# Performance work log

Hardware: AMD Instinct MI355X
Metric: run time of the kernel (lower is better)

The kernel has to match this reference:

```python
import jax, jax.numpy as jnp
import numpy as np

N, E, H, L = 2000, 32000, 300, 30


def setup_inputs() -> dict:
    key = jax.random.key(0)
    ks = jax.random.split(key, 24)
    x = jax.random.normal(ks[0], (N, 4), jnp.float32)
    edge_attr = jax.random.uniform(ks[1], (E, 2), dtype=jnp.float32)
    edge_index = jax.random.randint(ks[2], (2, E), 0, N, jnp.int32)
    y = jax.random.uniform(ks[3], (E,), dtype=jnp.float32)

    def w(k, shape, fan):
        return (jax.random.normal(k, shape, jnp.float32) / np.sqrt(fan)).astype(jnp.float32)

    inp = dict(x=x, edge_attr=edge_attr, edge_index=edge_index, y=y)
    inp['node_emb_W'] = w(ks[4], (4, H), 4)
    inp['node_emb_b'] = jnp.zeros((H,), jnp.float32)
    inp['edge_d_W'] = w(ks[5], (1, H // 2), 1)
    inp['edge_d_b'] = jnp.zeros((H // 2,), jnp.float32)
    inp['edge_t_W'] = w(ks[6], (1, H // 2), 1)
    inp['edge_t_b'] = jnp.zeros((H // 2,), jnp.float32)
    # stacked per-layer params [L, ...]
    inp['eU_W'] = w(ks[7], (L, H, H), H)
    inp['eU_b'] = jnp.zeros((L, H), jnp.float32)
    inp['eW_W'] = w(ks[8], (L, H, H), H)
    inp['eW_b'] = jnp.zeros((L, H), jnp.float32)
    inp['nU_W'] = w(ks[9], (L, H, H), H)
    inp['nU_b'] = jnp.zeros((L, H), jnp.float32)
    inp['nV_W'] = w(ks[10], (L, H, H), H)
    inp['nV_b'] = jnp.zeros((L, H), jnp.float32)
    inp['bn_e_g'] = jnp.ones((L, H), jnp.float32)
    inp['bn_e_b'] = jnp.zeros((L, H), jnp.float32)
    inp['bn_n_g'] = jnp.ones((L, H), jnp.float32)
    inp['bn_n_b'] = jnp.zeros((L, H), jnp.float32)
    inp['cls_W'] = w(ks[11], (H, 1), H)
    inp['cls_b'] = jnp.zeros((1,), jnp.float32)
    return inp


def _bn(v, g, b):  # BatchNorm1d in training mode (batch statistics), eps=1e-5
    m = v.mean(0)
    var = v.var(0)
    return (v - m) * jax.lax.rsqrt(var + 1e-5) * g + b


def _forward(x, edge_attr, edge_index, y, node_emb_W, node_emb_b, edge_d_W, edge_d_b,
             edge_t_W, edge_t_b, eU_W, eU_b, eW_W, eW_b, nU_W, nU_b, nV_W, nV_b,
             bn_e_g, bn_e_b, bn_n_g, bn_n_b, cls_W, cls_b):
    src, dst = edge_index[0], edge_index[1]
    n_nodes = x.shape[0]
    node = x @ node_emb_W + node_emb_b                                  # [N, H]
    edge = jnp.concatenate([edge_attr[:, :1] @ edge_d_W + edge_d_b,
                            edge_attr[:, 1:2] @ edge_t_W + edge_t_b], axis=1)  # [E, H]

    def layer(carry, p):
        node, edge = carry
        eUW, eUb, eWW, eWb, nUW, nUb, nVW, nVb, geg, geb, gng, gnb = p
        xs = node[src]                                                  # x_j gather [E, H]
        xd = node[dst]                                                  # x_i gather [E, H]
        # edge_update: edge_U(x_j) + edge_U(x_i)  (edge_U used for both, as in source)
        edge_gate = edge @ eWW + eWb + (xs @ eUW + eUb) + (xd @ eUW + eUb)
        edge_new = edge + jax.nn.relu(_bn(edge_gate, geg, geb))
        # message: eta * node_V(x_j), with global (dim=0) sigmoid-sum normalization as in source
        sigma = jax.nn.sigmoid(edge)
        eta = sigma / (sigma.sum(0) + 1e-20)                            # [E, H] / [H]
        msg = eta * (xs @ nVW + nVb)
        agg = jax.ops.segment_sum(msg, dst, num_segments=n_nodes)       # scatter-add
        node_gate = node @ nUW + nUb + agg
        node_new = node + jax.nn.relu(_bn(node_gate, gng, gnb))
        return (node_new, edge_new), None

    (node, edge), _ = jax.lax.scan(
        layer, (node, edge),
        (eU_W, eU_b, eW_W, eW_b, nU_W, nU_b, nV_W, nV_b, bn_e_g, bn_e_b, bn_n_g, bn_n_b))

    pred = jax.nn.sigmoid(edge @ cls_W + cls_b).reshape(-1)             # [E]
    pred_adj = jnp.zeros((n_nodes, n_nodes), pred.dtype).at[src, dst].add(pred)
    p = jnp.clip(pred, 1e-7, 1.0 - 1e-7)
    loss = -(y * jnp.log(p) + (1.0 - y) * jnp.log1p(-p)).mean()
    return pred_adj, loss


def reference(x, edge_attr, edge_index, y, node_emb_W, node_emb_b, edge_d_W, edge_d_b,
              edge_t_W, edge_t_b, eU_W, eU_b, eW_W, eW_b, nU_W, nU_b, nV_W, nV_b,
              bn_e_g, bn_e_b, bn_n_g, bn_n_b, cls_W, cls_b):
    return _forward(x, edge_attr, edge_index, y, node_emb_W, node_emb_b, edge_d_W,
                    edge_d_b, edge_t_W, edge_t_b, eU_W, eU_b, eW_W, eW_b, nU_W, nU_b,
                    nV_W, nV_b, bn_e_g, bn_e_b, bn_n_g, bn_n_b, cls_W, cls_b)
```

## Files before the change

kernel.cpp:

```cpp
#include <hip/hip_runtime.h>
#include <hip/hip_bf16.h>
#include <math.h>

#define N_NODES 2000
#define N_EDGES 32000
#define H 300
#define CH 75
#define HP 320
#define NLAYERS 30
#define NH (N_NODES * H)
#define NODE_ROWS_PAD 2048
#define WMAT (HP * HP)
#define NREP 32
#define RSTRIDE 608
#define SSTRIDE 304
#define NEB 500
#define NUB 147

typedef short bf16x8 __attribute__((ext_vector_type(8)));
typedef float f32x4 __attribute__((ext_vector_type(4)));
typedef __hip_bfloat16 bf16;

__device__ __forceinline__ float sigm(float x) { return 1.f / (1.f + __expf(-x)); }

__global__ __launch_bounds__(256) void zero_buf(float* __restrict__ p, int n) {
    int i = blockIdx.x * blockDim.x + threadIdx.x;
    if (i < n) p[i] = 0.f;
}

__global__ __launch_bounds__(256) void convert_weights_t(const float* __restrict__ eU,
                                                         const float* __restrict__ eW,
                                                         const float* __restrict__ nU,
                                                         const float* __restrict__ nV,
                                                         bf16* __restrict__ Wt) {
    __shared__ float tile[32][33];
    int b = blockIdx.x;
    int m = b / 100;
    int rem = b % 100;
    int kt = rem / 10, nt = rem % 10;
    int k0 = kt * 32, n0 = nt * 32;
    int grp = m / NLAYERS, l = m % NLAYERS;
    const float* S = (grp == 0) ? eU : (grp == 1) ? eW : (grp == 2) ? nU : nV;
    const float* Sl = S + (size_t)l * H * H;
    int t = threadIdx.x;
    int tn = t & 31, tk = t >> 5;
#pragma unroll
    for (int p = 0; p < 4; ++p) {
        int k = tk + p * 8;
        int gk = k0 + k, gn = n0 + tn;
        tile[k][tn] = (gk < H && gn < H) ? Sl[(size_t)gk * H + gn] : 0.f;
    }
    __syncthreads();
    bf16* D = Wt + (size_t)m * WMAT;
    int tk2 = t & 31, tn2 = t >> 5;
#pragma unroll
    for (int p = 0; p < 4; ++p) {
        int n = tn2 + p * 8;
        D[(size_t)(n0 + n) * HP + k0 + tk2] = __float2bfloat16(tile[tk2][n]);
    }
}

__global__ __launch_bounds__(256) void convert_wtk(const bf16* __restrict__ Wt,
                                                   bf16* __restrict__ WtK) {
    long long idx = (long long)blockIdx.x * 256 + threadIdx.x;
    if (idx >= 30LL * WMAT) return;
    int m = (int)(idx / WMAT);
    int rem = (int)(idx % WMAT);
    int ct4 = rem / 25600;
    int r2 = rem % 25600;
    int kc = r2 / 640;
    int r3 = r2 % 640;
    int c = r3 / 8, j = r3 % 8;
    WtK[idx] = Wt[(size_t)(30 + m) * WMAT + (size_t)(ct4 * 80 + c) * HP + kc * 8 + j];
}

__global__ __launch_bounds__(256) void csr_hist(const int* __restrict__ dst,
                                                int* __restrict__ counts) {
    int i = blockIdx.x * 256 + threadIdx.x;
    if (i < N_EDGES) atomicAdd(&counts[dst[i]], 1);
}

__global__ __launch_bounds__(256) void csr_scan(const int* __restrict__ counts,
                                                int* __restrict__ offs,
                                                int* __restrict__ woff) {
    __shared__ int part[256];
    int t = threadIdx.x;
    int base = t * 8;
    int local[8];
    int s = 0;
#pragma unroll
    for (int j = 0; j < 8; ++j) {
        int c = (base + j < N_NODES) ? counts[base + j] : 0;
        local[j] = s;
        s += c;
    }
    part[t] = s;
    __syncthreads();
    for (int off = 1; off < 256; off <<= 1) {
        int v = (t >= off) ? part[t - off] : 0;
        __syncthreads();
        part[t] += v;
        __syncthreads();
    }
    int pre = (t == 0) ? 0 : part[t - 1];
#pragma unroll
    for (int j = 0; j < 8; ++j) {
        int idx = base + j;
        if (idx < N_NODES) { int v = pre + local[j]; offs[idx] = v; woff[idx] = v; }
    }
    if (t == 255) offs[N_NODES] = part[255];
}

__global__ __launch_bounds__(256) void csr_scatter(const int* __restrict__ src,
                                                   const int* __restrict__ dst,
                                                   int* __restrict__ woff,
                                                   int* __restrict__ eidx,
                                                   int* __restrict__ msrc) {
    int i = blockIdx.x * 256 + threadIdx.x;
    if (i < N_EDGES) {
        int p = atomicAdd(&woff[dst[i]], 1);
        eidx[p] = i;
        msrc[p] = src[i];
    }
}

__global__ __launch_bounds__(256) void node_embed(const float* __restrict__ x,
                                                  const float* __restrict__ W,
                                                  const float* __restrict__ b,
                                                  float* __restrict__ node,
                                                  bf16* __restrict__ node_bf) {
    int i = blockIdx.x * blockDim.x + threadIdx.x;
    if (i >= NH) return;
    int n = i / H, h = i % H;
    float acc = b[h];
#pragma unroll
    for (int k = 0; k < 4; ++k) acc += x[n * 4 + k] * W[k * H + h];
    node[i] = acc;
    node_bf[(size_t)n * HP + h] = __float2bfloat16(acc);
}

__global__ __launch_bounds__(256) void edge_embed(const float* __restrict__ ea,
                                                  const float* __restrict__ dW,
                                                  const float* __restrict__ db,
                                                  const float* __restrict__ tW,
                                                  const float* __restrict__ tb,
                                                  bf16* __restrict__ edge_bf,
                                                  float* __restrict__ RS0) {
    __shared__ float s_s[SSTRIDE];
    int t = threadIdx.x;
    for (int i = t; i < SSTRIDE; i += 256) s_s[i] = 0.f;
    __syncthreads();
    int hc = t % 80, rgrp = t / 80;
    int col0 = hc * 4;
    float ss[4] = {0.f, 0.f, 0.f, 0.f};
    if (hc < CH && rgrp < 3) {
        float wv[4], bv[4];
#pragma unroll
        for (int j = 0; j < 4; ++j) {
            int col = col0 + j;
            wv[j] = (col < 150) ? dW[col] : tW[col - 150];
            bv[j] = (col < 150) ? db[col] : tb[col - 150];
        }
        int e0 = blockIdx.x * 64;
        for (int r = rgrp; r < 64; r += 3) {
            int e = e0 + r;
            float d = ea[2 * e], tt = ea[2 * e + 1];
            union { ushort4 u; bf16 b[4]; } ob;
#pragma unroll
            for (int j = 0; j < 4; ++j) {
                int col = col0 + j;
                float v = ((col < 150) ? d : tt) * wv[j] + bv[j];
                ob.b[j] = __float2bfloat16(v);
                ss[j] += sigm(__bfloat162float(ob.b[j]));
            }
            *(ushort4*)(edge_bf + (size_t)e * HP + col0) = ob.u;
        }
#pragma unroll
        for (int j = 0; j < 4; ++j) atomicAdd(&s_s[col0 + j], ss[j]);
    }
    __syncthreads();
    float* rs = RS0 + (size_t)(blockIdx.x & (NREP - 1)) * SSTRIDE;
    for (int i = t; i < H; i += 256) atomicAdd(&rs[i], s_s[i]);
}

__global__ __launch_bounds__(64) void gemm_node(const bf16* __restrict__ node_bf,
                                                const bf16* __restrict__ Wt_all,
                                                const float* __restrict__ eU_b,
                                                const float* __restrict__ nV_b,
                                                const float* __restrict__ nU_b,
                                                int layer,
                                                float* __restrict__ nodeU,
                                                float* __restrict__ nodeV,
                                                float* __restrict__ nodeUn,
                                                const float* __restrict__ RScur,
                                                float* __restrict__ RSnxt,
                                                float* __restrict__ invS) {
    int bx = blockIdx.x;
    int lane = threadIdx.x;
    if (bx >= 1500) {
        int idx = bx - 1500;
        int c = idx * 64 + lane;
        if (c < H) {
            float ssr = 0.f;
#pragma unroll 8
            for (int r = 0; r < NREP; ++r) ssr += RScur[r * SSTRIDE + c];
            invS[c] = 1.f / (ssr + 1e-20f);
        }
        for (int i = idx * 64 + lane; i < NREP * SSTRIDE; i += 320) RSnxt[i] = 0.f;
        return;
    }
    int mat = bx / 500;
    int rem = bx % 500;
    int rt0 = rem >> 2, ct4 = rem & 3;
    const bf16* Bt; const float* bias; float* out;
    if (mat == 0)      { Bt = Wt_all + (size_t)(0 + layer) * WMAT;  bias = eU_b + layer * H; out = nodeU; }
    else if (mat == 1) { Bt = Wt_all + (size_t)(90 + layer) * WMAT; bias = nV_b + layer * H; out = nodeV; }
    else               { Bt = Wt_all + (size_t)(60 + layer) * WMAT; bias = nU_b + layer * H; out = nodeUn; }
    int row0 = rt0 * 16, c0 = ct4 * 80;
    int rlo = lane & 15, khi = lane >> 4;
    f32x4 acc[5];
#pragma unroll
    for (int ct = 0; ct < 5; ++ct) acc[ct] = (f32x4)0.f;
#pragma unroll 2
    for (int ks = 0; ks < 10; ++ks) {
        int kk = ks * 32 + khi * 8;
        bf16x8 a, b[5];
        a = *(const bf16x8*)(node_bf + (size_t)(row0 + rlo) * HP + kk);
#pragma unroll
        for (int ct = 0; ct < 5; ++ct)
            b[ct] = *(const bf16x8*)(Bt + (size_t)(c0 + ct * 16 + rlo) * HP + kk);
#pragma unroll
        for (int ct = 0; ct < 5; ++ct)
            acc[ct] = __builtin_amdgcn_mfma_f32_16x16x32_bf16(a, b[ct], acc[ct], 0, 0, 0);
    }
    int rhi = lane >> 4;
#pragma unroll
    for (int ct = 0; ct < 5; ++ct) {
        int col = c0 + ct * 16 + rlo;
        if (col >= H) continue;
        float bv = bias[col];
#pragma unroll
        for (int j = 0; j < 4; ++j) {
            int r = row0 + rhi * 4 + j;
            out[(size_t)r * H + col] = acc[ct][j] + bv;
        }
    }
}

__global__ __launch_bounds__(256) void gemm_edge(const bf16* __restrict__ edge_bf,
                                                 const bf16* __restrict__ WtK_l,
                                                 const float* __restrict__ nodeU,
                                                 const int* __restrict__ src,
                                                 const int* __restrict__ dst,
                                                 bf16* __restrict__ gate_bf,
                                                 float* __restrict__ REc) {
    __shared__ bf16 smA[32 * 320];
    int tid = threadIdx.x;
    int bx = blockIdx.x;
    int wave = tid >> 6, lane = tid & 63;
    int row0 = bx * 32;
    int c0 = wave * 80;
    int rlo = lane & 15, khi = lane >> 4, rhi = lane >> 4;

    int se_[8], de_[8];
#pragma unroll
    for (int rt = 0; rt < 2; ++rt)
#pragma unroll
        for (int j = 0; j < 4; ++j) {
            int r = row0 + rt * 16 + rhi * 4 + j;
            se_[rt * 4 + j] = src[r];
            de_[rt * 4 + j] = dst[r];
        }

    const uint4* Ag = (const uint4*)(edge_bf + (size_t)row0 * HP);
#pragma unroll
    for (int it = 0; it < 5; ++it) {
        int cid = it * 256 + tid;
        int row = cid / 40, ch = cid % 40;
        uint4 v = Ag[cid];
        *(uint4*)(smA + row * 320 + ((ch ^ (row & 7)) << 3)) = v;
    }
    __syncthreads();

    const bf16* Bw = WtK_l + (size_t)wave * 25600;
    f32x4 acc[2][5];
#pragma unroll
    for (int rt = 0; rt < 2; ++rt)
#pragma unroll
        for (int ct = 0; ct < 5; ++ct) acc[rt][ct] = (f32x4)0.f;
#pragma unroll 2
    for (int ks = 0; ks < 10; ++ks) {
        int c = ks * 4 + khi;
        int kcb = (ks * 4 + khi) * 80;
        bf16x8 a[2], b[5];
#pragma unroll
        for (int rt = 0; rt < 2; ++rt) {
            int row = rt * 16 + rlo;
            a[rt] = *(const bf16x8*)(smA + row * 320 + ((c ^ (row & 7)) << 3));
        }
#pragma unroll
        for (int ct = 0; ct < 5; ++ct)
            b[ct] = *(const bf16x8*)(Bw + (size_t)(kcb + ct * 16 + rlo) * 8);
#pragma unroll
        for (int rt = 0; rt < 2; ++rt)
#pragma unroll
            for (int ct = 0; ct < 5; ++ct)
                acc[rt][ct] = __builtin_amdgcn_mfma_f32_16x16x32_bf16(a[rt], b[ct], acc[rt][ct], 0, 0, 0);
    }
    float csum[5], csq[5];
#pragma unroll
    for (int ct = 0; ct < 5; ++ct) { csum[ct] = 0.f; csq[ct] = 0.f; }
#pragma unroll
    for (int rt = 0; rt < 2; ++rt)
#pragma unroll
        for (int j = 0; j < 4; ++j) {
            int r = row0 + rt * 16 + rhi * 4 + j;
            int se = se_[rt * 4 + j], de = de_[rt * 4 + j];
#pragma unroll
            for (int ct = 0; ct < 5; ++ct) {
                int col = c0 + ct * 16 + rlo;
                if (col < H) {
                    float g = acc[rt][ct][j] + nodeU[(size_t)se * H + col] + nodeU[(size_t)de * H + col];
                    gate_bf[(size_t)r * H + col] = __float2bfloat16(g);
                    csum[ct] += g;
                    csq[ct] += g * g;
                }
            }
        }
#pragma unroll
    for (int ct = 0; ct < 5; ++ct) {
        csum[ct] += __shfl_xor(csum[ct], 16, 64);
        csum[ct] += __shfl_xor(csum[ct], 32, 64);
        csq[ct]  += __shfl_xor(csq[ct], 16, 64);
        csq[ct]  += __shfl_xor(csq[ct], 32, 64);
    }
    if (khi == 0) {
        float* re = REc + (size_t)(bx & (NREP - 1)) * RSTRIDE;
#pragma unroll
        for (int ct = 0; ct < 5; ++ct) {
            int col = c0 + ct * 16 + rlo;
            if (col < H) {
                atomicAdd(&re[col], csum[ct]);
                atomicAdd(&re[SSTRIDE + col], csq[ct]);
            }
        }
    }
}

__global__ __launch_bounds__(320) void node_msg(const bf16* __restrict__ edge_bf,
                                                const float* __restrict__ nodeV,
                                                const float* __restrict__ nodeUn,
                                                const int* __restrict__ offs,
                                                const int* __restrict__ eidx,
                                                const int* __restrict__ msrc,
                                                const float* __restrict__ invS,
                                                float* __restrict__ RN,
                                                float* __restrict__ aggv) {
    int t = threadIdx.x;
    int bx = blockIdx.x;
    if (t >= H) return;
    float inv = invS[t];
    float st1 = 0.f, st2 = 0.f;
    int n0 = bx * 2;
#pragma unroll
    for (int k = 0; k < 2; ++k) {
        int n = n0 + k;
        int beg = offs[n], end = offs[n + 1];
        float a = 0.f;
        for (int i = beg; i < end; ++i) {
            int e = eidx[i];
            int s = msrc[i];
            a += sigm(__bfloat162float(edge_bf[(size_t)e * HP + t])) * nodeV[(size_t)s * H + t];
        }
        float v = nodeUn[(size_t)n * H + t] + a * inv;
        aggv[(size_t)n * H + t] = v;
        st1 += v; st2 += v * v;
    }
    float* rn = RN + (size_t)(bx & (NREP - 1)) * RSTRIDE;
    atomicAdd(&rn[t], st1);
    atomicAdd(&rn[SSTRIDE + t], st2);
}

__global__ __launch_bounds__(256) void fused_final(bf16* __restrict__ edge_bf,
                                                   const bf16* __restrict__ gate_bf,
                                                   const float* __restrict__ REc,
                                                   float* __restrict__ REo,
                                                   const float* __restrict__ RNc,
                                                   float* __restrict__ RNo,
                                                   float* __restrict__ RSnext,
                                                   const float* __restrict__ eg,
                                                   const float* __restrict__ ebt,
                                                   const float* __restrict__ ng,
                                                   const float* __restrict__ nbt,
                                                   float* __restrict__ node,
                                                   bf16* __restrict__ node_bf,
                                                   const float* __restrict__ aggv) {
    __shared__ float sc_s[SSTRIDE], of_s[SSTRIDE], s_s[SSTRIDE];
    int bx = blockIdx.x, t = threadIdx.x;
    if (bx < NEB) {
        const float invE = 1.f / N_EDGES;
        for (int i = t; i < SSTRIDE; i += 256) {
            s_s[i] = 0.f;
            if (i < H) {
                float gs = 0.f, gq = 0.f;
#pragma unroll 8
                for (int r = 0; r < NREP; ++r) {
                    gs += REc[r * RSTRIDE + i];
                    gq += REc[r * RSTRIDE + SSTRIDE + i];
                }
                float mean = gs * invE;
                float var = fmaxf(gq * invE - mean * mean, 0.f);
                float rstd = rsqrtf(var + 1e-5f);
                float sc = rstd * eg[i];
                sc_s[i] = sc;
                of_s[i] = ebt[i] - mean * sc;
            }
        }
        __syncthreads();
        int hc = t % 80, rgrp = t / 80;
        bool act = (hc < CH) && (rgrp < 3);
        float ss[4] = {0.f, 0.f, 0.f, 0.f};
        int col0 = hc * 4;
        if (act) {
            float sc[4], of[4];
#pragma unroll
            for (int j = 0; j < 4; ++j) { sc[j] = sc_s[col0 + j]; of[j] = of_s[col0 + j]; }
            int e0 = bx * 64;
            for (int r = rgrp; r < 64; r += 3) {
                int e = e0 + r;
                union { ushort4 u; bf16 b[4]; } eb, gv, ob;
                eb.u = *(const ushort4*)(edge_bf + (size_t)e * HP + col0);
                gv.u = *(const ushort4*)(gate_bf + (size_t)e * H + col0);
#pragma unroll
                for (int j = 0; j < 4; ++j) {
                    float g = __bfloat162float(gv.b[j]);
                    float val = fmaxf(fmaf(g, sc[j], of[j]), 0.f);
                    float nv = __bfloat162float(eb.b[j]) + val;
                    ob.b[j] = __float2bfloat16(nv);
                    ss[j] += sigm(__bfloat162float(ob.b[j]));
                }
                *(ushort4*)(edge_bf + (size_t)e * HP + col0) = ob.u;
            }
#pragma unroll
            for (int j = 0; j < 4; ++j) atomicAdd(&s_s[col0 + j], ss[j]);
        }
        __syncthreads();
        float* rs = RSnext + (size_t)(bx & (NREP - 1)) * SSTRIDE;
        for (int i = t; i < H; i += 256) atomicAdd(&rs[i], s_s[i]);
    } else {
        int idx = bx - NEB;
        if (idx < NREP) {
            for (int i = t; i < RSTRIDE; i += 256) {
                REo[(size_t)idx * RSTRIDE + i] = 0.f;
                RNo[(size_t)idx * RSTRIDE + i] = 0.f;
            }
        }
        const float invN = 1.f / N_NODES;
        for (int i = t; i < H; i += 256) {
            float ns = 0.f, nq = 0.f;
#pragma unroll 8
            for (int r = 0; r < NREP; ++r) {
                ns += RNc[r * RSTRIDE + i];
                nq += RNc[r * RSTRIDE + SSTRIDE + i];
            }
            float mean = ns * invN;
            float var = fmaxf(nq * invN - mean * mean, 0.f);
            float rstd = rsqrtf(var + 1e-5f);
            float sc = rstd * ng[i];
            sc_s[i] = sc;
            of_s[i] = nbt[i] - mean * sc;
        }
        __syncthreads();
#pragma unroll
        for (int it = 0; it < 4; ++it) {
            int c = idx * 1024 + it * 256 + t;
            if (c >= NH / 4) break;
            int n = c / CH, hc = c % CH, col0 = hc * 4;
            float4 v4 = ((const float4*)aggv)[c];
            float4 nd = ((const float4*)node)[c];
            const float* v4p = (const float*)&v4;
            const float* ndp = (const float*)&nd;
            union { ushort4 u; bf16 b[4]; } ob;
            float outv[4];
#pragma unroll
            for (int j = 0; j < 4; ++j) {
                float g = fmaf(v4p[j], sc_s[col0 + j], of_s[col0 + j]);
                outv[j] = ndp[j] + fmaxf(g, 0.f);
                ob.b[j] = __float2bfloat16(outv[j]);
            }
            ((float4*)node)[c] = make_float4(outv[0], outv[1], outv[2], outv[3]);
            *(ushort4*)(node_bf + (size_t)n * HP + col0) = ob.u;
        }
    }
}

__global__ __launch_bounds__(256) void classify_loss(const bf16* __restrict__ edge_bf,
                                                     const float* __restrict__ clsW,
                                                     const float* __restrict__ clsb,
                                                     const int* __restrict__ src,
                                                     const int* __restrict__ dst,
                                                     const float* __restrict__ y,
                                                     float* __restrict__ out) {
    __shared__ float wl[4];
    int lane = threadIdx.x & 63;
    int wid = threadIdx.x >> 6;
    int quad = lane >> 2;
    int ql = lane & 3;
    float w[80];
#pragma unroll
    for (int j = 0; j < 80; ++j) {
        int col = ql * 80 + j;
        w[j] = (col < H) ? clsW[col] : 0.f;
    }
    int g = blockIdx.x * 4 + wid;
    int e = g * 16 + quad;
    const bf16* row = edge_bf + (size_t)e * HP + ql * 80;
    float acc = 0.f;
#pragma unroll
    for (int v = 0; v < 10; ++v) {
        bf16x8 bv = *(const bf16x8*)(row + v * 8);
#pragma unroll
        for (int j = 0; j < 8; ++j)
            acc += __bfloat162float(((const bf16*)&bv)[j]) * w[v * 8 + j];
    }
    acc += __shfl_xor(acc, 1, 64);
    acc += __shfl_xor(acc, 2, 64);
    float lsum = 0.f;
    if (ql == 0) {
        float z = acc + clsb[0];
        float p = 1.f / (1.f + __expf(-z));
        atomicAdd(&out[(size_t)src[e] * N_NODES + dst[e]], p);
        float pc = fminf(fmaxf(p, 1e-7f), 1.f - 1e-7f);
        lsum = -(y[e] * __logf(pc) + (1.f - y[e]) * log1pf(-pc));
    }
#pragma unroll
    for (int off = 32; off > 0; off >>= 1) lsum += __shfl_down(lsum, off, 64);
    if (lane == 0) wl[wid] = lsum;
    __syncthreads();
    if (threadIdx.x == 0) {
        float tt = wl[0] + wl[1] + wl[2] + wl[3];
        atomicAdd(&out[(size_t)N_NODES * N_NODES], tt * (1.f / N_EDGES));
    }
}

extern "C" void kernel_launch(void* const* d_in, const int* in_sizes, int n_in,
                              void* d_out, int out_size, void* d_ws, size_t ws_size,
                              hipStream_t stream) {
    const float* x          = (const float*)d_in[0];
    const float* edge_attr  = (const float*)d_in[1];
    const int*   edge_index = (const int*)d_in[2];
    const float* y          = (const float*)d_in[3];
    const float* node_emb_W = (const float*)d_in[4];
    const float* node_emb_b = (const float*)d_in[5];
    const float* edge_d_W   = (const float*)d_in[6];
    const float* edge_d_b   = (const float*)d_in[7];
    const float* edge_t_W   = (const float*)d_in[8];
    const float* edge_t_b   = (const float*)d_in[9];
    const float* eU_W = (const float*)d_in[10];
    const float* eU_b = (const float*)d_in[11];
    const float* eW_W = (const float*)d_in[12];
    const float* nU_W = (const float*)d_in[14];
    const float* nU_b = (const float*)d_in[15];
    const float* nV_W = (const float*)d_in[16];
    const float* nV_b = (const float*)d_in[17];
    const float* bn_e_g = (const float*)d_in[18];
    const float* bn_e_b = (const float*)d_in[19];
    const float* bn_n_g = (const float*)d_in[20];
    const float* bn_n_b = (const float*)d_in[21];
    const float* cls_W = (const float*)d_in[22];
    const float* cls_b = (const float*)d_in[23];

    const int* src = edge_index;
    const int* dst = edge_index + N_EDGES;

    float* ws     = (float*)d_ws;
    float* node   = ws;
    float* nodeU  = node + NH;
    float* nodeV  = nodeU + NH;
    float* nodeUn = nodeV + NH;
    float* aggv   = nodeUn + NH;
    float* RE2    = aggv + NH;
    float* RN2    = RE2 + 2 * NREP * RSTRIDE;
    float* RS2    = RN2 + 2 * NREP * RSTRIDE;
    float* invS   = RS2 + 2 * NREP * SSTRIDE;
    bf16* node_bf = (bf16*)(invS + SSTRIDE);
    bf16* edge_bf = node_bf + (size_t)NODE_ROWS_PAD * HP;
    bf16* gate_bf = edge_bf + (size_t)N_EDGES * HP;
    bf16* Wt_all  = gate_bf + (size_t)N_EDGES * H;
    bf16* WtK_all = Wt_all + (size_t)120 * WMAT;
    int* csr_counts = (int*)(WtK_all + (size_t)30 * WMAT);
    int* csr_offs   = csr_counts + 2048;
    int* csr_woff   = csr_offs + 2048;
    int* csr_eidx   = csr_woff + 2048;
    int* csr_msrc   = csr_eidx + N_EDGES;

    float* out = (float*)d_out;

    int zstats = 4 * NREP * RSTRIDE + 2 * NREP * SSTRIDE + SSTRIDE;
    int zlen = zstats + (NODE_ROWS_PAD * HP + N_EDGES * HP) / 2;
    zero_buf<<<(N_NODES * N_NODES + 1 + 255) / 256, 256, 0, stream>>>(out, N_NODES * N_NODES + 1);
    zero_buf<<<(zlen + 255) / 256, 256, 0, stream>>>(RE2, zlen);
    zero_buf<<<8, 256, 0, stream>>>((float*)csr_counts, 2048);

    convert_weights_t<<<12000, 256, 0, stream>>>(eU_W, eW_W, nU_W, nV_W, Wt_all);
    convert_wtk<<<(30 * WMAT + 255) / 256, 256, 0, stream>>>(Wt_all, WtK_all);
    csr_hist<<<(N_EDGES + 255) / 256, 256, 0, stream>>>(dst, csr_counts);
    csr_scan<<<1, 256, 0, stream>>>(csr_counts, csr_offs, csr_woff);
    csr_scatter<<<(N_EDGES + 255) / 256, 256, 0, stream>>>(src, dst, csr_woff, csr_eidx, csr_msrc);
    node_embed<<<(NH + 255) / 256, 256, 0, stream>>>(x, node_emb_W, node_emb_b, node, node_bf);
    edge_embed<<<NEB, 256, 0, stream>>>(edge_attr, edge_d_W, edge_d_b,
                                        edge_t_W, edge_t_b, edge_bf, RS2);

    for (int l = 0; l < NLAYERS; ++l) {
        float* REc = RE2 + (size_t)(l & 1) * NREP * RSTRIDE;
        float* REo = RE2 + (size_t)((l + 1) & 1) * NREP * RSTRIDE;
        float* RNc = RN2 + (size_t)(l & 1) * NREP * RSTRIDE;
        float* RNo = RN2 + (size_t)((l + 1) & 1) * NREP * RSTRIDE;
        float* RScur = RS2 + (size_t)(l & 1) * NREP * SSTRIDE;
        float* RSnxt = RS2 + (size_t)((l + 1) & 1) * NREP * SSTRIDE;
        const bf16* WtK_l = WtK_all + (size_t)l * WMAT;

        gemm_node<<<1505, 64, 0, stream>>>(node_bf, Wt_all, eU_b, nV_b, nU_b, l,
                                           nodeU, nodeV, nodeUn, RScur, RSnxt, invS);
        gemm_edge<<<1000, 256, 0, stream>>>(edge_bf, WtK_l, nodeU, src, dst,
                                            gate_bf, REc);
        node_msg<<<N_NODES / 2, 320, 0, stream>>>(edge_bf, nodeV, nodeUn,
                                                  csr_offs, csr_eidx, csr_msrc,
                                                  invS, RNc, aggv);
        fused_final<<<NEB + NUB, 256, 0, stream>>>(edge_bf, gate_bf,
                                                   REc, REo, RNc, RNo, RSnxt,
                                                   bn_e_g + l * H, bn_e_b + l * H,
                                                   bn_n_g + l * H, bn_n_b + l * H,
                                                   node, node_bf, aggv);
    }

    classify_loss<<<500, 256, 0, stream>>>(edge_bf, cls_W, cls_b, src, dst, y, out);
}
```

Before: 2.546 ms.

## Fuse edge GEMM with node message aggregation and pre-tile all weights

Merges the per-layer edge GEMM and node message-aggregation kernels into one launch, where blocks 0-999 do the edge GEMM and blocks 1000-1999 do the node aggregation. This removes one launch per layer and lets the two independent stages overlap on the GPU. The weight conversion now writes all four weight groups directly into the k-chunked layout, so the separate conversion pass goes away and gemm_node reads the same layout with contiguous B loads. The fused kernel runs node work on 256 threads with two columns per thread, and the heterogeneous blocks may raise register pressure for the node path.

Result: faster. 2.407 ms (-5.5%).

```diff
diff --git a/kernel.cpp b/kernel.cpp
--- a/kernel.cpp
+++ b/kernel.cpp
@@ -28,11 +28,11 @@
     if (i < n) p[i] = 0.f;
 }
 
-__global__ __launch_bounds__(256) void convert_weights_t(const float* __restrict__ eU,
+__global__ __launch_bounds__(256) void convert_weights_k(const float* __restrict__ eU,
                                                          const float* __restrict__ eW,
                                                          const float* __restrict__ nU,
                                                          const float* __restrict__ nV,
-                                                         bf16* __restrict__ Wt) {
+                                                         bf16* __restrict__ WtK) {
     __shared__ float tile[32][33];
     int b = blockIdx.x;
     int m = b / 100;
@@ -51,27 +51,16 @@
         tile[k][tn] = (gk < H && gn < H) ? Sl[(size_t)gk * H + gn] : 0.f;
     }
     __syncthreads();
-    bf16* D = Wt + (size_t)m * WMAT;
-    int tk2 = t & 31, tn2 = t >> 5;
+    bf16* D = WtK + (size_t)m * WMAT;
+    int nn = t >> 3, j8 = t & 7;
+    int n = n0 + nn;
+    int ct4 = n / 80, c = n % 80;
 #pragma unroll
     for (int p = 0; p < 4; ++p) {
-        int n = tn2 + p * 8;
-        D[(size_t)(n0 + n) * HP + k0 + tk2] = __float2bfloat16(tile[tk2][n]);
-    }
-}
-
-__global__ __launch_bounds__(256) void convert_wtk(const bf16* __restrict__ Wt,
-                                                   bf16* __restrict__ WtK) {
-    long long idx = (long long)blockIdx.x * 256 + threadIdx.x;
-    if (idx >= 30LL * WMAT) return;
-    int m = (int)(idx / WMAT);
-    int rem = (int)(idx % WMAT);
-    int ct4 = rem / 25600;
-    int r2 = rem % 25600;
-    int kc = r2 / 640;
-    int r3 = r2 % 640;
-    int c = r3 / 8, j = r3 % 8;
-    WtK[idx] = Wt[(size_t)(30 + m) * WMAT + (size_t)(ct4 * 80 + c) * HP + kc * 8 + j];
+        int kc = (k0 >> 3) + p;
+        D[(size_t)ct4 * 25600 + (size_t)kc * 640 + c * 8 + j8] =
+            __float2bfloat16(tile[p * 8 + j8][nn]);
+    }
 }
 
 __global__ __launch_bounds__(256) void csr_hist(const int* __restrict__ dst,
@@ -184,7 +173,7 @@
 }
 
 __global__ __launch_bounds__(64) void gemm_node(const bf16* __restrict__ node_bf,
-                                                const bf16* __restrict__ Wt_all,
+                                                const bf16* __restrict__ WtK_all,
                                                 const float* __restrict__ eU_b,
                                                 const float* __restrict__ nV_b,
                                                 const float* __restrict__ nU_b,
@@ -212,10 +201,11 @@
     int mat = bx / 500;
     int rem = bx % 500;
     int rt0 = rem >> 2, ct4 = rem & 3;
-    const bf16* Bt; const float* bias; float* out;
-    if (mat == 0)      { Bt = Wt_all + (size_t)(0 + layer) * WMAT;  bias = eU_b + layer * H; out = nodeU; }
-    else if (mat == 1) { Bt = Wt_all + (size_t)(90 + layer) * WMAT; bias = nV_b + layer * H; out = nodeV; }
-    else               { Bt = Wt_all + (size_t)(60 + layer) * WMAT; bias = nU_b + layer * H; out = nodeUn; }
+    int m; const float* bias; float* out;
+    if (mat == 0)      { m = layer;      bias = eU_b + layer * H; out = nodeU; }
+    else if (mat == 1) { m = 90 + layer; bias = nV_b + layer * H; out = nodeV; }
+    else               { m = 60 + layer; bias = nU_b + layer * H; out = nodeUn; }
+    const bf16* Bw = WtK_all + (size_t)m * WMAT + (size_t)ct4 * 25600;
     int row0 = rt0 * 16, c0 = ct4 * 80;
     int rlo = lane & 15, khi = lane >> 4;
     f32x4 acc[5];
@@ -224,11 +214,12 @@
 #pragma unroll 2
     for (int ks = 0; ks < 10; ++ks) {
         int kk = ks * 32 + khi * 8;
+        int kcb = (ks * 4 + khi) * 80;
         bf16x8 a, b[5];
         a = *(const bf16x8*)(node_bf + (size_t)(row0 + rlo) * HP + kk);
 #pragma unroll
         for (int ct = 0; ct < 5; ++ct)
-            b[ct] = *(const bf16x8*)(Bt + (size_t)(c0 + ct * 16 + rlo) * HP + kk);
+            b[ct] = *(const bf16x8*)(Bw + (size_t)(kcb + ct * 16 + rlo) * 8);
 #pragma unroll
         for (int ct = 0; ct < 5; ++ct)
             acc[ct] = __builtin_amdgcn_mfma_f32_16x16x32_bf16(a, b[ct], acc[ct], 0, 0, 0);
@@ -247,138 +238,153 @@
     }
 }
 
-__global__ __launch_bounds__(256) void gemm_edge(const bf16* __restrict__ edge_bf,
+__global__ __launch_bounds__(256) void fused_mid(const bf16* __restrict__ edge_bf,
                                                  const bf16* __restrict__ WtK_l,
                                                  const float* __restrict__ nodeU,
                                                  const int* __restrict__ src,
                                                  const int* __restrict__ dst,
                                                  bf16* __restrict__ gate_bf,
-                                                 float* __restrict__ REc) {
+                                                 float* __restrict__ REc,
+                                                 const float* __restrict__ nodeV,
+                                                 const float* __restrict__ nodeUn,
+                                                 const int* __restrict__ offs,
+                                                 const int* __restrict__ eidx,
+                                                 const int* __restrict__ msrc,
+                                                 const float* __restrict__ invS,
+                                                 float* __restrict__ RNc,
+                                                 float* __restrict__ aggv) {
     __shared__ bf16 smA[32 * 320];
     int tid = threadIdx.x;
     int bx = blockIdx.x;
-    int wave = tid >> 6, lane = tid & 63;
-    int row0 = bx * 32;
-    int c0 = wave * 80;
-    int rlo = lane & 15, khi = lane >> 4, rhi = lane >> 4;
-
-    int se_[8], de_[8];
-#pragma unroll
-    for (int rt = 0; rt < 2; ++rt)
-#pragma unroll
-        for (int j = 0; j < 4; ++j) {
-            int r = row0 + rt * 16 + rhi * 4 + j;
-            se_[rt * 4 + j] = src[r];
-            de_[rt * 4 + j] = dst[r];
-        }
-
-    const uint4* Ag = (const uint4*)(edge_bf + (size_t)row0 * HP);
-#pragma unroll
-    for (int it = 0; it < 5; ++it) {
-        int cid = it * 256 + tid;
-        int row = cid / 40, ch = cid % 40;
-        uint4 v = Ag[cid];
-        *(uint4*)(smA + row * 320 + ((ch ^ (row & 7)) << 3)) = v;
-    }
-    __syncthreads();
-
-    const bf16* Bw = WtK_l + (size_t)wave * 25600;
-    f32x4 acc[2][5];
-#pragma unroll
-    for (int rt = 0; rt < 2; ++rt)
-#pragma unroll
-        for (int ct = 0; ct < 5; ++ct) acc[rt][ct] = (f32x4)0.f;
+    if (bx < 1000) {
+        int wave = tid >> 6, lane = tid & 63;
+        int row0 = bx * 32;
+        int c0 = wave * 80;
+        int rlo = lane & 15, khi = lane >> 4, rhi = lane >> 4;
+
+        int se_[8], de_[8];
+#pragma unroll
+        for (int rt = 0; rt < 2; ++rt)
+#pragma unroll
+            for (int j = 0; j < 4; ++j) {
+                int r = row0 + rt * 16 + rhi * 4 + j;
+                se_[rt * 4 + j] = src[r];
+                de_[rt * 4 + j] = dst[r];
+            }
+
+        const uint4* Ag = (const uint4*)(edge_bf + (size_t)row0 * HP);
+#pragma unroll
+        for (int it = 0; it < 5; ++it) {
+            int cid = it * 256 + tid;
+            int row = cid / 40, ch = cid % 40;
+            uint4 v = Ag[cid];
+            *(uint4*)(smA + row * 320 + ((ch ^ (row & 7)) << 3)) = v;
+        }
+        __syncthreads();
+
+        const bf16* Bw = WtK_l + (size_t)wave * 25600;
+        f32x4 acc[2][5];
+#pragma unroll
+        for (int rt = 0; rt < 2; ++rt)
+#pragma unroll
+            for (int ct = 0; ct < 5; ++ct) acc[rt][ct] = (f32x4)0.f;
 #pragma unroll 2
-    for (int ks = 0; ks < 10; ++ks) {
-        int c = ks * 4 + khi;
-        int kcb = (ks * 4 + khi) * 80;
-        bf16x8 a[2], b[5];
-#pragma unroll
-        for (int rt = 0; rt < 2; ++rt) {
-            int row = rt * 16 + rlo;
-            a[rt] = *(const bf16x8*)(smA + row * 320 + ((c ^ (row & 7)) << 3));
-        }
-#pragma unroll
-        for (int ct = 0; ct < 5; ++ct)
-            b[ct] = *(const bf16x8*)(Bw + (size_t)(kcb + ct * 16 + rlo) * 8);
+        for (int ks = 0; ks < 10; ++ks) {
+            int c = ks * 4 + khi;
+            int kcb = (ks * 4 + khi) * 80;
+            bf16x8 a[2], b[5];
+#pragma unroll
+            for (int rt = 0; rt < 2; ++rt) {
+                int row = rt * 16 + rlo;
+                a[rt] = *(const bf16x8*)(smA + row * 320 + ((c ^ (row & 7)) << 3));
+            }
+#pragma unroll
+            for (int ct = 0; ct < 5; ++ct)
+                b[ct] = *(const bf16x8*)(Bw + (size_t)(kcb + ct * 16 + rlo) * 8);
+#pragma unroll
+            for (int rt = 0; rt < 2; ++rt)
+#pragma unroll
+                for (int ct = 0; ct < 5; ++ct)
+                    acc[rt][ct] = __builtin_amdgcn_mfma_f32_16x16x32_bf16(a[rt], b[ct], acc[rt][ct], 0, 0, 0);
+        }
+        float csum[5], csq[5];
+#pragma unroll
+        for (int ct = 0; ct < 5; ++ct) { csum[ct] = 0.f; csq[ct] = 0.f; }
 #pragma unroll
         for (int rt = 0; rt < 2; ++rt)
 #pragma unroll
-            for (int ct = 0; ct < 5; ++ct)
-                acc[rt][ct] = __builtin_amdgcn_mfma_f32_16x16x32_bf16(a[rt], b[ct], acc[rt][ct], 0, 0, 0);
-    }
-    float csum[5], csq[5];
-#pragma unroll
-    for (int ct = 0; ct < 5; ++ct) { csum[ct] = 0.f; csq[ct] = 0.f; }
-#pragma unroll
-    for (int rt = 0; rt < 2; ++rt)
-#pragma unroll
-        for (int j = 0; j < 4; ++j) {
-            int r = row0 + rt * 16 + rhi * 4 + j;
-            int se = se_[rt * 4 + j], de = de_[rt * 4 + j];
+            for (int j = 0; j < 4; ++j) {
+                int r = row0 + rt * 16 + rhi * 4 + j;
+                int se = se_[rt * 4 + j], de = de_[rt * 4 + j];
+#pragma unroll
+                for (int ct = 0; ct < 5; ++ct) {
+                    int col = c0 + ct * 16 + rlo;
+                    if (col < H) {
+                        float g = acc[rt][ct][j] + nodeU[(size_t)se * H + col] + nodeU[(size_t)de * H + col];
+                        gate_bf[(size_t)r * H + col] = __float2bfloat16(g);
+                        csum[ct] += g;
+                        csq[ct] += g * g;
+                    }
+                }
+            }
+#pragma unroll
+        for (int ct = 0; ct < 5; ++ct) {
+            csum[ct] += __shfl_xor(csum[ct], 16, 64);
+            csum[ct] += __shfl_xor(csum[ct], 32, 64);
+            csq[ct]  += __shfl_xor(csq[ct], 16, 64);
+            csq[ct]  += __shfl_xor(csq[ct], 32, 64);
+        }
+        if (khi == 0) {
+            float* re = REc + (size_t)(bx & (NREP - 1)) * RSTRIDE;
 #pragma unroll
             for (int ct = 0; ct < 5; ++ct) {
                 int col = c0 + ct * 16 + rlo;
                 if (col < H) {
-                    float g = acc[rt][ct][j] + nodeU[(size_t)se * H + col] + nodeU[(size_t)de * H + col];
-                    gate_bf[(size_t)r * H + col] = __float2bfloat16(g);
-                    csum[ct] += g;
-                    csq[ct] += g * g;
+                    atomicAdd(&re[col], csum[ct]);
+                    atomicAdd(&re[SSTRIDE + col], csq[ct]);
                 }
             }
         }
-#pragma unroll
-    for (int ct = 0; ct < 5; ++ct) {
-        csum[ct] += __shfl_xor(csum[ct], 16, 64);
-        csum[ct] += __shfl_xor(csum[ct], 32, 64);
-        csq[ct]  += __shfl_xor(csq[ct], 16, 64);
-        csq[ct]  += __shfl_xor(csq[ct], 32, 64);
-    }
-    if (khi == 0) {
-        float* re = REc + (size_t)(bx & (NREP - 1)) * RSTRIDE;
-#pragma unroll
-        for (int ct = 0; ct < 5; ++ct) {
-            int col = c0 + ct * 16 + rlo;
-            if (col < H) {
-                atomicAdd(&re[col], csum[ct]);
-                atomicAdd(&re[SSTRIDE + col], csq[ct]);
-            }
-        }
-    }
-}
-
-__global__ __launch_bounds__(320) void node_msg(const bf16* __restrict__ edge_bf,
-                                                const float* __restrict__ nodeV,
-                                                const float* __restrict__ nodeUn,
-                                                const int* __restrict__ offs,
-                                                const int* __restrict__ eidx,
-                                                const int* __restrict__ msrc,
-                                                const float* __restrict__ invS,
-                                                float* __restrict__ RN,
-                                                float* __restrict__ aggv) {
-    int t = threadIdx.x;
-    int bx = blockIdx.x;
-    if (t >= H) return;
-    float inv = invS[t];
-    float st1 = 0.f, st2 = 0.f;
-    int n0 = bx * 2;
-#pragma unroll
-    for (int k = 0; k < 2; ++k) {
-        int n = n0 + k;
-        int beg = offs[n], end = offs[n + 1];
-        float a = 0.f;
-        for (int i = beg; i < end; ++i) {
-            int e = eidx[i];
-            int s = msrc[i];
-            a += sigm(__bfloat162float(edge_bf[(size_t)e * HP + t])) * nodeV[(size_t)s * H + t];
-        }
-        float v = nodeUn[(size_t)n * H + t] + a * inv;
-        aggv[(size_t)n * H + t] = v;
-        st1 += v; st2 += v * v;
-    }
-    float* rn = RN + (size_t)(bx & (NREP - 1)) * RSTRIDE;
-    atomicAdd(&rn[t], st1);
-    atomicAdd(&rn[SSTRIDE + t], st2);
+    } else {
+        int nb = bx - 1000;
+        int h0 = tid;
+        bool has1 = (tid < H - 256);
+        int h1 = 256 + tid;
+        float inv0 = invS[h0];
+        float inv1 = has1 ? invS[h1] : 0.f;
+        float st10 = 0.f, st20 = 0.f, st11 = 0.f, st21 = 0.f;
+        int n0 = nb * 2;
+#pragma unroll
+        for (int k = 0; k < 2; ++k) {
+            int n = n0 + k;
+            int beg = offs[n], end = offs[n + 1];
+            float a0 = 0.f, a1 = 0.f;
+            for (int i = beg; i < end; ++i) {
+                int e = eidx[i];
+                int s = msrc[i];
+                const bf16* er = edge_bf + (size_t)e * HP;
+                const float* vr = nodeV + (size_t)s * H;
+                a0 += sigm(__bfloat162float(er[h0])) * vr[h0];
+                if (has1) a1 += sigm(__bfloat162float(er[h1])) * vr[h1];
+            }
+            size_t nbase = (size_t)n * H;
+            float v0 = nodeUn[nbase + h0] + a0 * inv0;
+            aggv[nbase + h0] = v0;
+            st10 += v0; st20 += v0 * v0;
+            if (has1) {
+                float v1 = nodeUn[nbase + h1] + a1 * inv1;
+                aggv[nbase + h1] = v1;
+                st11 += v1; st21 += v1 * v1;
+            }
+        }
+        float* rn = RNc + (size_t)(nb & (NREP - 1)) * RSTRIDE;
+        atomicAdd(&rn[h0], st10);
+        atomicAdd(&rn[SSTRIDE + h0], st20);
+        if (has1) {
+            atomicAdd(&rn[h1], st11);
+            atomicAdd(&rn[SSTRIDE + h1], st21);
+        }
+    }
 }
 
 __global__ __launch_bounds__(256) void fused_final(bf16* __restrict__ edge_bf,
@@ -586,9 +592,8 @@
     bf16* node_bf = (bf16*)(invS + SSTRIDE);
     bf16* edge_bf = node_bf + (size_t)NODE_ROWS_PAD * HP;
     bf16* gate_bf = edge_bf + (size_t)N_EDGES * HP;
-    bf16* Wt_all  = gate_bf + (size_t)N_EDGES * H;
-    bf16* WtK_all = Wt_all + (size_t)120 * WMAT;
-    int* csr_counts = (int*)(WtK_all + (size_t)30 * WMAT);
+    bf16* WtK_all = gate_bf + (size_t)N_EDGES * H;
+    int* csr_counts = (int*)(WtK_all + (size_t)120 * WMAT);
     int* csr_offs   = csr_counts + 2048;
     int* csr_woff   = csr_offs + 2048;
     int* csr_eidx   = csr_woff + 2048;
@@ -602,8 +607,7 @@
     zero_buf<<<(zlen + 255) / 256, 256, 0, stream>>>(RE2, zlen);
     zero_buf<<<8, 256, 0, stream>>>((float*)csr_counts, 2048);
 
-    convert_weights_t<<<12000, 256, 0, stream>>>(eU_W, eW_W, nU_W, nV_W, Wt_all);
-    convert_wtk<<<(30 * WMAT + 255) / 256, 256, 0, stream>>>(Wt_all, WtK_all);
+    convert_weights_k<<<12000, 256, 0, stream>>>(eU_W, eW_W, nU_W, nV_W, WtK_all);
     csr_hist<<<(N_EDGES + 255) / 256, 256, 0, stream>>>(dst, csr_counts);
     csr_scan<<<1, 256, 0, stream>>>(csr_counts, csr_offs, csr_woff);
     csr_scatter<<<(N_EDGES + 255) / 256, 256, 0, stream>>>(src, dst, csr_woff, csr_eidx, csr_msrc);
@@ -618,15 +622,14 @@
         float* RNo = RN2 + (size_t)((l + 1) & 1) * NREP * RSTRIDE;
         float* RScur = RS2 + (size_t)(l & 1) * NREP * SSTRIDE;
         float* RSnxt = RS2 + (size_t)((l + 1) & 1) * NREP * SSTRIDE;
-        const bf16* WtK_l = WtK_all + (size_t)l * WMAT;
-
-        gemm_node<<<1505, 64, 0, stream>>>(node_bf, Wt_all, eU_b, nV_b, nU_b, l,
+        const bf16* WtK_e = WtK_all + (size_t)(30 + l) * WMAT;
+
+        gemm_node<<<1505, 64, 0, stream>>>(node_bf, WtK_all, eU_b, nV_b, nU_b, l,
                                            nodeU, nodeV, nodeUn, RScur, RSnxt, invS);
-        gemm_edge<<<1000, 256, 0, stream>>>(edge_bf, WtK_l, nodeU, src, dst,
-                                            gate_bf, REc);
-        node_msg<<<N_NODES / 2, 320, 0, stream>>>(edge_bf, nodeV, nodeUn,
-                                                  csr_offs, csr_eidx, csr_msrc,
-                                                  invS, RNc, aggv);
+        fused_mid<<<2000, 256, 0, stream>>>(edge_bf, WtK_e, nodeU, src, dst,
+                                            gate_bf, REc,
+                                            nodeV, nodeUn, csr_offs, csr_eidx, csr_msrc,
+                                            invS, RNc, aggv);
         fused_final<<<NEB + NUB, 256, 0, stream>>>(edge_bf, gate_bf,
                                                    REc, REo, RNc, RNo, RSnxt,
                                                    bn_e_g + l * H, bn_e_b + l * H,
```
